# Performance work log

Hardware: AMD Instinct MI355X
Metric: run time of the kernel (lower is better)

The kernel has to match this reference:

```python
import jax, jax.numpy as jnp
import numpy as np

E, K, D_IN, D_OUT, D_HID = 16, 2, 1024, 1024, 2048

def setup_inputs() -> dict:
    key = jax.random.key(0)
    ks = jax.random.split(key, 6)
    s_in = 1.0 / np.sqrt(D_IN)
    s_hid = 1.0 / np.sqrt(D_HID)
    return {
        "x": jax.random.normal(ks[0], (4096, D_IN), dtype=jnp.float32),
        "gate_w": jax.random.uniform(ks[1], (E, D_IN), jnp.float32, -s_in, s_in),
        "w1": jax.random.uniform(ks[2], (E, D_HID, D_IN), jnp.float32, -s_in, s_in),
        "b1": jax.random.uniform(ks[3], (E, D_HID), jnp.float32, -s_in, s_in),
        "w2": jax.random.uniform(ks[4], (E, D_OUT, D_HID), jnp.float32, -s_hid, s_hid),
        "b2": jax.random.uniform(ks[5], (E, D_OUT), jnp.float32, -s_hid, s_hid),
    }

def reference(x, gate_w, w1, b1, w2, b2):
    # gate: [B, E]
    gate_scores = jnp.einsum('bi,ei->be', x, gate_w)
    topk_vals, topk_idxs = jax.lax.top_k(gate_scores, K)  # [B, K]
    topk_weights = jax.nn.softmax(topk_vals, axis=-1)     # [B, K]
    # dense all-expert MLP (faithful to reference): [B, E, D_OUT]
    h = jax.nn.relu(jnp.einsum('bi,ehi->beh', x, w1) + b1[None])
    expert_outputs = jnp.einsum('beh,eoh->beo', h, w2) + b2[None]
    # gather selected experts: [B, K, D_OUT]
    sel = jnp.take_along_axis(expert_outputs, topk_idxs[:, :, None], axis=1)
    return jnp.sum(sel * topk_weights[:, :, None], axis=1)
```

## Files before the change

### kernel.cpp

```cpp
#include <hip/hip_runtime.h>
#include <hip/hip_bf16.h>
#include <math.h>

#define B_TOK 4096
#define NE 16
#define DI 1024
#define DH 2048
#define DOUT 1024
#define NSLOT (B_TOK * 2)

typedef unsigned short u16;
typedef short bfrag __attribute__((ext_vector_type(8)));
typedef float f32x4 __attribute__((ext_vector_type(4)));
typedef u16 u16x8 __attribute__((ext_vector_type(8)));

__device__ __forceinline__ u16 f2bf(float f) {
    union { float f; unsigned u; } v; v.f = f;
    return (u16)((v.u + 0x7fffu + ((v.u >> 16) & 1u)) >> 16);
}

__device__ __forceinline__ void async16(const void* g, void* lds) {
    __builtin_amdgcn_global_load_lds(
        (const __attribute__((address_space(1))) void*)g,
        (__attribute__((address_space(3))) void*)lds,
        16, 0, 0);
}

__global__ void zero_init(float* __restrict__ out, int n4) {
    int i = blockIdx.x * blockDim.x + threadIdx.x;
    if (i < n4) ((float4*)out)[i] = make_float4(0.f, 0.f, 0.f, 0.f);
}

__global__ void convert_bf16(const float* __restrict__ src, u16* __restrict__ dst, int n8) {
    int i = blockIdx.x * blockDim.x + threadIdx.x;
    if (i >= n8) return;
    const float4* s4 = (const float4*)src;
    float4 a = s4[2 * i], b = s4[2 * i + 1];
    u16x8 r;
    r[0] = f2bf(a.x); r[1] = f2bf(a.y); r[2] = f2bf(a.z); r[3] = f2bf(a.w);
    r[4] = f2bf(b.x); r[5] = f2bf(b.y); r[6] = f2bf(b.z); r[7] = f2bf(b.w);
    ((u16x8*)dst)[i] = r;
}

__global__ __launch_bounds__(256) void gate_topk(
    const float* __restrict__ x, const float* __restrict__ gw,
    int* __restrict__ token_e, float* __restrict__ token_w)
{
    int wave = threadIdx.x >> 6, lane = threadIdx.x & 63;
    int t = blockIdx.x * 4 + wave;
    const float4* x4 = (const float4*)(x + (size_t)t * DI);
    const float4* g4 = (const float4*)gw;
    double acc[NE];
#pragma unroll
    for (int e = 0; e < NE; ++e) acc[e] = 0.0;
#pragma unroll
    for (int i = 0; i < 4; ++i) {
        float4 xv = x4[lane + i * 64];
#pragma unroll
        for (int e = 0; e < NE; ++e) {
            float4 gv = g4[e * 256 + lane + i * 64];
            acc[e] += (double)xv.x * gv.x + (double)xv.y * gv.y
                    + (double)xv.z * gv.z + (double)xv.w * gv.w;
        }
    }
#pragma unroll
    for (int e = 0; e < NE; ++e) {
        double v = acc[e];
        for (int off = 32; off; off >>= 1) v += __shfl_xor(v, off, 64);
        acc[e] = v;
    }
    if (lane == 0) {
        int e0 = 0; double v0 = acc[0];
#pragma unroll
        for (int e = 1; e < NE; ++e) if (acc[e] > v0) { v0 = acc[e]; e0 = e; }
        int e1 = -1; double v1 = -1e300;
#pragma unroll
        for (int e = 0; e < NE; ++e) if (e != e0 && acc[e] > v1) { v1 = acc[e]; e1 = e; }
        float d = expf((float)(v1 - v0));
        float w0 = 1.f / (1.f + d);
        float w1 = d * w0;
        token_e[2 * t] = e0; token_e[2 * t + 1] = e1;
        token_w[2 * t] = w0; token_w[2 * t + 1] = w1;
    }
}

__global__ __launch_bounds__(1024) void route(
    const int* __restrict__ token_e, const float* __restrict__ token_w,
    int* __restrict__ counts, int* __restrict__ offsets,
    int* __restrict__ slot_token, float* __restrict__ slot_wgt)
{
    __shared__ int lcnt[NE];
    __shared__ int lcur[NE];
    int tid = threadIdx.x;
    if (tid < NE) lcnt[tid] = 0;
    __syncthreads();
    for (int i = tid; i < NSLOT; i += 1024) atomicAdd(&lcnt[token_e[i]], 1);
    __syncthreads();
    if (tid == 0) {
        int s = 0;
        for (int e = 0; e < NE; ++e) {
            int c = lcnt[e];
            counts[e] = c; offsets[e] = s; lcur[e] = s; s += c;
        }
    }
    __syncthreads();
    for (int i = tid; i < NSLOT; i += 1024) {
        int e = token_e[i];
        int pos = atomicAdd(&lcur[e], 1);
        slot_token[pos] = i >> 1;
        slot_wgt[pos] = token_w[i];
    }
}

template <int PHASE>
__global__ __launch_bounds__(256) void moe_gemm(
    const u16* __restrict__ Abuf,
    const u16* __restrict__ Bbuf,
    const float* __restrict__ bias,
    const int* __restrict__ counts, const int* __restrict__ offsets,
    const int* __restrict__ slot_token, const float* __restrict__ slot_wgt,
    u16* __restrict__ hb, float* __restrict__ out)
{
    constexpr int KDIM = (PHASE == 1) ? DI : DH;
    constexpr int NDIM = (PHASE == 1) ? DH : DOUT;

    const int e = blockIdx.z;
    const int cnt = counts[e];
    const int m0 = blockIdx.y * 128;
    if (m0 >= cnt) return;
    const int n0 = blockIdx.x * 128;
    const int sbase = offsets[e];

    __shared__ u16 ldsbuf[8192];
    u16* alds = ldsbuf;
    u16* blds = ldsbuf + 4096;

    const int tid = threadIdx.x;
    const int wv = tid >> 6, lane = tid & 63;
    const int lrow = lane >> 2, lkc = lane & 3;

    const int arow0 = wv * 16 + lrow;
    const int arow1 = 64 + wv * 16 + lrow;

    const u16* aptr0; const u16* aptr1;
    if (PHASE == 1) {
        int c = cnt - 1;
        int r0 = m0 + arow0; if (r0 > c) r0 = c;
        int r1 = m0 + arow1; if (r1 > c) r1 = c;
        aptr0 = Abuf + (size_t)slot_token[sbase + r0] * KDIM + lkc * 8;
        aptr1 = Abuf + (size_t)slot_token[sbase + r1] * KDIM + lkc * 8;
    } else {
        int s0 = sbase + m0 + arow0; if (s0 > NSLOT - 1) s0 = NSLOT - 1;
        int s1 = sbase + m0 + arow1; if (s1 > NSLOT - 1) s1 = NSLOT - 1;
        aptr0 = Abuf + (size_t)s0 * KDIM + lkc * 8;
        aptr1 = Abuf + (size_t)s1 * KDIM + lkc * 8;
    }
    const u16* bbase = Bbuf + (size_t)e * NDIM * KDIM;
    const u16* bptr0 = bbase + (size_t)(n0 + arow0) * KDIM + lkc * 8;
    const u16* bptr1 = bbase + (size_t)(n0 + arow1) * KDIM + lkc * 8;

    u16* alds_w0 = alds + wv * 512;
    u16* alds_w1 = alds + 2048 + wv * 512;
    u16* blds_w0 = blds + wv * 512;
    u16* blds_w1 = blds + 2048 + wv * 512;

    f32x4 acc[4][4];
#pragma unroll
    for (int i = 0; i < 4; ++i)
#pragma unroll
        for (int j = 0; j < 4; ++j) acc[i][j] = (f32x4){0.f, 0.f, 0.f, 0.f};

    const int wm = (wv & 1) * 64, wn = (wv >> 1) * 64;
    const int quad = lane >> 4, mr = lane & 15;
    const int aoff = (wm + mr) * 32 + quad * 8;
    const int boff = (wn + mr) * 32 + quad * 8;

    const int nk = KDIM / 32;
    for (int kt = 0; kt < nk; ++kt) {
        __syncthreads();
        async16(aptr0 + kt * 32, alds_w0);
        async16(aptr1 + kt * 32, alds_w1);
        async16(bptr0 + kt * 32, blds_w0);
        async16(bptr1 + kt * 32, blds_w1);
        __syncthreads();
        bfrag af[4], bf[4];
#pragma unroll
        for (int i = 0; i < 4; ++i) af[i] = *(const bfrag*)(alds + aoff + i * 512);
#pragma unroll
        for (int j = 0; j < 4; ++j) bf[j] = *(const bfrag*)(blds + boff + j * 512);
#pragma unroll
        for (int i = 0; i < 4; ++i)
#pragma unroll
            for (int j = 0; j < 4; ++j)
                acc[i][j] = __builtin_amdgcn_mfma_f32_16x16x32_bf16(af[i], bf[j], acc[i][j], 0, 0, 0);
    }

    const float* bias_e = bias + e * NDIM;
    if constexpr (PHASE == 1) {
#pragma unroll
        for (int i = 0; i < 4; ++i) {
            int mbase = wm + i * 16 + quad * 4;
#pragma unroll
            for (int j = 0; j < 4; ++j) {
                int n = n0 + wn + j * 16 + mr;
                float bv = bias_e[n];
#pragma unroll
                for (int r = 0; r < 4; ++r) {
                    int m = m0 + mbase + r;
                    if (m < cnt) {
                        float v = acc[i][j][r] + bv;
                        v = v > 0.f ? v : 0.f;
                        hb[(size_t)(sbase + m) * DH + n] = f2bf(v);
                    }
                }
            }
        }
    } else {
#pragma unroll
        for (int i = 0; i < 4; ++i) {
            int mbase = wm + i * 16 + quad * 4;
#pragma unroll
            for (int r = 0; r < 4; ++r) {
                int m = m0 + mbase + r;
                if (m < cnt) {
                    int slot = sbase + m;
                    int tok = slot_token[slot];
                    float wgt = slot_wgt[slot];
                    float* orow = out + (size_t)tok * DOUT + n0 + wn;
#pragma unroll
                    for (int j = 0; j < 4; ++j) {
                        int nl = j * 16 + mr;
                        float v = wgt * (acc[i][j][r] + bias_e[n0 + wn + nl]);
                        atomicAdd(orow + nl, v);
                    }
                }
            }
        }
    }
}

extern "C" void kernel_launch(void* const* d_in, const int* in_sizes, int n_in,
                              void* d_out, int out_size, void* d_ws, size_t ws_size,
                              hipStream_t stream) {
    const float* x  = (const float*)d_in[0];
    const float* gw = (const float*)d_in[1];
    const float* w1 = (const float*)d_in[2];
    const float* b1 = (const float*)d_in[3];
    const float* w2 = (const float*)d_in[4];
    const float* b2 = (const float*)d_in[5];
    float* out = (float*)d_out;

    char* ws = (char*)d_ws;
    u16* xb = (u16*)ws;
    u16* wb = (u16*)(ws + 8388608);
    u16* hb = (u16*)(ws + 8388608 + 67108864);
    char* rb = ws + 109051904;
    int*   counts     = (int*)(rb);
    int*   offsets    = (int*)(rb + 64);
    int*   token_e    = (int*)(rb + 192);
    float* token_w    = (float*)(rb + 192 + 32768);
    int*   slot_token = (int*)(rb + 192 + 65536);
    float* slot_wgt   = (float*)(rb + 192 + 98304);

    zero_init<<<4096, 256, 0, stream>>>(out, (B_TOK * DOUT) / 4);
    convert_bf16<<<2048, 256, 0, stream>>>(x, xb, (B_TOK * DI) / 8);
    convert_bf16<<<16384, 256, 0, stream>>>(w1, wb, (NE * DH * DI) / 8);
    gate_topk<<<1024, 256, 0, stream>>>(x, gw, token_e, token_w);
    route<<<1, 1024, 0, stream>>>(token_e, token_w, counts, offsets, slot_token, slot_wgt);
    moe_gemm<1><<<dim3(DH / 128, B_TOK / 128, NE), 256, 0, stream>>>(
        xb, wb, b1, counts, offsets, slot_token, slot_wgt, hb, out);
    convert_bf16<<<16384, 256, 0, stream>>>(w2, wb, (NE * DOUT * DH) / 8);
    moe_gemm<2><<<dim3(DOUT / 128, B_TOK / 128, NE), 256, 0, stream>>>(
        hb, wb, b2, counts, offsets, slot_token, slot_wgt, hb, out);
}
```

Baseline: 515.1 us.

## Double K-tile depth to 64 and XOR-swizzle LDS layout in MoE GEMM

Raises the K step per loop iteration from 32 to 64, so each tile load covers twice the data and the number of barrier pairs is halved. The 16-byte chunk placement in LDS is XOR-swizzled by row, and fragment reads are swizzled to match, to avoid LDS bank conflicts with the wider 128-byte rows. LDS use per block doubles to 32 KB, which may lower occupancy.

```diff
diff --git a/kernel.cpp b/kernel.cpp
--- a/kernel.cpp
+++ b/kernel.cpp
@@ -131,38 +131,31 @@
     const int n0 = blockIdx.x * 128;
     const int sbase = offsets[e];
 
-    __shared__ u16 ldsbuf[8192];
+    __shared__ u16 ldsbuf[16384];
     u16* alds = ldsbuf;
-    u16* blds = ldsbuf + 4096;
+    u16* blds = ldsbuf + 8192;
 
     const int tid = threadIdx.x;
     const int wv = tid >> 6, lane = tid & 63;
-    const int lrow = lane >> 2, lkc = lane & 3;
-
-    const int arow0 = wv * 16 + lrow;
-    const int arow1 = 64 + wv * 16 + lrow;
-
-    const u16* aptr0; const u16* aptr1;
-    if (PHASE == 1) {
-        int c = cnt - 1;
-        int r0 = m0 + arow0; if (r0 > c) r0 = c;
-        int r1 = m0 + arow1; if (r1 > c) r1 = c;
-        aptr0 = Abuf + (size_t)slot_token[sbase + r0] * KDIM + lkc * 8;
-        aptr1 = Abuf + (size_t)slot_token[sbase + r1] * KDIM + lkc * 8;
-    } else {
-        int s0 = sbase + m0 + arow0; if (s0 > NSLOT - 1) s0 = NSLOT - 1;
-        int s1 = sbase + m0 + arow1; if (s1 > NSLOT - 1) s1 = NSLOT - 1;
-        aptr0 = Abuf + (size_t)s0 * KDIM + lkc * 8;
-        aptr1 = Abuf + (size_t)s1 * KDIM + lkc * 8;
-    }
+    const int lrow = lane >> 3;
+    const int lkc = lane & 7;
+    const int skc = lkc ^ lrow;
+
+    const u16* aptr[4]; const u16* bptr[4];
     const u16* bbase = Bbuf + (size_t)e * NDIM * KDIM;
-    const u16* bptr0 = bbase + (size_t)(n0 + arow0) * KDIM + lkc * 8;
-    const u16* bptr1 = bbase + (size_t)(n0 + arow1) * KDIM + lkc * 8;
-
-    u16* alds_w0 = alds + wv * 512;
-    u16* alds_w1 = alds + 2048 + wv * 512;
-    u16* blds_w0 = blds + wv * 512;
-    u16* blds_w1 = blds + 2048 + wv * 512;
+#pragma unroll
+    for (int r = 0; r < 4; ++r) {
+        int arow = m0 + r * 32 + wv * 8 + lrow;
+        if (PHASE == 1) {
+            int c = cnt - 1; if (arow > c) arow = c;
+            aptr[r] = Abuf + (size_t)slot_token[sbase + arow] * KDIM + skc * 8;
+        } else {
+            int s = sbase + arow; if (s > NSLOT - 1) s = NSLOT - 1;
+            aptr[r] = Abuf + (size_t)s * KDIM + skc * 8;
+        }
+        int brow = n0 + r * 32 + wv * 8 + lrow;
+        bptr[r] = bbase + (size_t)brow * KDIM + skc * 8;
+    }
 
     f32x4 acc[4][4];
 #pragma unroll
@@ -172,27 +165,31 @@
 
     const int wm = (wv & 1) * 64, wn = (wv >> 1) * 64;
     const int quad = lane >> 4, mr = lane & 15;
-    const int aoff = (wm + mr) * 32 + quad * 8;
-    const int boff = (wn + mr) * 32 + quad * 8;
-
-    const int nk = KDIM / 32;
+    const int msw = mr & 7;
+
+    const int nk = KDIM / 64;
     for (int kt = 0; kt < nk; ++kt) {
         __syncthreads();
-        async16(aptr0 + kt * 32, alds_w0);
-        async16(aptr1 + kt * 32, alds_w1);
-        async16(bptr0 + kt * 32, blds_w0);
-        async16(bptr1 + kt * 32, blds_w1);
+#pragma unroll
+        for (int r = 0; r < 4; ++r) {
+            async16(aptr[r] + kt * 64, alds + (r * 32 + wv * 8) * 64);
+            async16(bptr[r] + kt * 64, blds + (r * 32 + wv * 8) * 64);
+        }
         __syncthreads();
-        bfrag af[4], bf[4];
-#pragma unroll
-        for (int i = 0; i < 4; ++i) af[i] = *(const bfrag*)(alds + aoff + i * 512);
-#pragma unroll
-        for (int j = 0; j < 4; ++j) bf[j] = *(const bfrag*)(blds + boff + j * 512);
-#pragma unroll
-        for (int i = 0; i < 4; ++i)
-#pragma unroll
-            for (int j = 0; j < 4; ++j)
-                acc[i][j] = __builtin_amdgcn_mfma_f32_16x16x32_bf16(af[i], bf[j], acc[i][j], 0, 0, 0);
+#pragma unroll
+        for (int kk = 0; kk < 2; ++kk) {
+            bfrag af[4], bf[4];
+            const int ch = ((kk * 4 + quad) ^ msw) * 8;
+#pragma unroll
+            for (int i = 0; i < 4; ++i) af[i] = *(const bfrag*)(alds + (wm + i * 16 + mr) * 64 + ch);
+#pragma unroll
+            for (int j = 0; j < 4; ++j) bf[j] = *(const bfrag*)(blds + (wn + j * 16 + mr) * 64 + ch);
+#pragma unroll
+            for (int i = 0; i < 4; ++i)
+#pragma unroll
+                for (int j = 0; j < 4; ++j)
+                    acc[i][j] = __builtin_amdgcn_mfma_f32_16x16x32_bf16(af[i], bf[j], acc[i][j], 0, 0, 0);
+        }
     }
 
     const float* bias_e = bias + e * NDIM;
```

After: 567.4 us. 1.1x slower.
